# Kernel optimization log

Hardware: AMD Instinct MI355X
Metric: run time of the kernel (lower is better)

## Reference

```python
import jax, jax.numpy as jnp
import numpy as np

B, L, D, H, PD = 1, 512, 1024, 16, 128
HW = D // H  # 64


def _layernorm(x, g, b, eps=1e-5):
    mu = jnp.mean(x, axis=-1, keepdims=True)
    var = jnp.var(x, axis=-1, keepdims=True)
    return (x - mu) * jax.lax.rsqrt(var + eps) * g + b


def setup_inputs() -> dict:
    key = jax.random.key(0)
    ks = jax.random.split(key, 16)
    s = 0.02
    return {
        "sequence_state": jax.random.normal(ks[0], (B, L, D), jnp.float32),
        "pairwise_state": jax.random.normal(ks[1], (B, L, L, PD), jnp.float32),
        "mask": jnp.ones((B, L), dtype=bool),
        # layernorm before attention
        "ln1_g": jnp.ones((D,), jnp.float32),
        "ln1_b": jnp.zeros((D,), jnp.float32),
        # attention params (weights stored [in, out])
        "proj_w": jax.random.normal(ks[2], (D, 3 * H * HW), jnp.float32) * s,
        "g_w": jax.random.normal(ks[3], (D, H * HW), jnp.float32) * s,
        "g_b": jnp.ones((H * HW,), jnp.float32),
        "o_w": jax.random.normal(ks[4], (H * HW, D), jnp.float32) * s,
        "o_b": jnp.zeros((D,), jnp.float32),
        # pair-to-sequence bias
        "p2s_ln_g": jnp.ones((PD,), jnp.float32),
        "p2s_ln_b": jnp.zeros((PD,), jnp.float32),
        "p2s_w": jax.random.normal(ks[5], (PD, H), jnp.float32) * s,
        # residue MLP
        "mlp_ln_g": jnp.ones((D,), jnp.float32),
        "mlp_ln_b": jnp.zeros((D,), jnp.float32),
        "mlp_w1": jax.random.normal(ks[6], (D, 4 * D), jnp.float32) * s,
        "mlp_b1": jnp.zeros((4 * D,), jnp.float32),
        "mlp_w2": jax.random.normal(ks[7], (4 * D, D), jnp.float32) * s,
        "mlp_b2": jnp.zeros((D,), jnp.float32),
    }


def reference(sequence_state, pairwise_state, mask,
              ln1_g, ln1_b, proj_w, g_w, g_b, o_w, o_b,
              p2s_ln_g, p2s_ln_b, p2s_w,
              mlp_ln_g, mlp_ln_b, mlp_w1, mlp_b1, mlp_w2, mlp_b2):
    # PairToSequence: LN over pairwise feature dim, then project to per-head bias
    z = _layernorm(pairwise_state, p2s_ln_g, p2s_ln_b)
    bias = jnp.einsum("bqkp,ph->bhqk", z, p2s_w)  # [B,H,L,L]

    # Pre-attention layernorm
    y = _layernorm(sequence_state, ln1_g, ln1_b)

    # Gated attention with pairwise bias
    t = (y @ proj_w).reshape(B, L, H, 3 * HW)
    q, k, v = jnp.split(t, 3, axis=-1)  # each [B,L,H,HW]
    q = q * (HW ** -0.5)
    a = jnp.einsum("bqhc,bkhc->bhqk", q, k) + bias
    a = jnp.where(mask[:, None, None, :], a, -jnp.inf)
    a = jax.nn.softmax(a, axis=-1)
    o = jnp.einsum("bhqk,bkhc->bqhc", a, v).reshape(B, L, H * HW)
    gate = jax.nn.sigmoid(y @ g_w + g_b)
    o = (gate * o) @ o_w + o_b

    # residual (dropout=0 -> identity)
    s = sequence_state + o

    # ResidueMLP: x + Linear(ReLU(Linear(LN(x))))
    h = _layernorm(s, mlp_ln_g, mlp_ln_b)
    h = jax.nn.relu(h @ mlp_w1 + mlp_b1) @ mlp_w2 + mlp_b2
    return s + h
```

## Files before the change

kernel.cpp:

```cpp
#include <hip/hip_runtime.h>


typedef __attribute__((ext_vector_type(8))) short bfrag;
typedef __attribute__((ext_vector_type(4))) float f32x4;
typedef unsigned short ushort_t;
typedef unsigned int u32;

#define AS1 __attribute__((address_space(1)))
#define AS3 __attribute__((address_space(3)))

__device__ __forceinline__ void gll16(const void* g, void* l) {
  __builtin_amdgcn_global_load_lds((const AS1 u32*)g, (AS3 u32*)l, 16, 0, 0);
}

__device__ __forceinline__ unsigned short f2b(float x) {
  union { float f; unsigned u; } a; a.f = x;
  unsigned r = a.u + 0x7fffu + ((a.u >> 16) & 1u);
  return (unsigned short)(r >> 16);
}
__device__ __forceinline__ unsigned pack2(float a, float b) {
  return (unsigned)f2b(a) | ((unsigned)f2b(b) << 16);
}
__device__ __forceinline__ float b2f(ushort_t u) {
  union { float f; unsigned v; } a; a.v = ((unsigned)u) << 16; return a.f;
}

#define OFF_BIASH ((size_t)0)
#define OFF_Y     ((size_t)8388608)
#define OFF_QS    (OFF_Y    + (size_t)1048576)
#define OFF_KS    (OFF_QS   + (size_t)1048576)
#define OFF_VT    (OFF_KS   + (size_t)1048576)
#define OFF_GATE  (OFF_VT   + (size_t)1048576)
#define OFF_OG    (OFF_GATE + (size_t)2097152)
#define OFF_S     (OFF_OG   + (size_t)1048576)
#define OFF_HLN   (OFF_S    + (size_t)2097152)
#define OFF_H1    (OFF_HLN  + (size_t)1048576)
#define OFF_WPG   (OFF_H1   + (size_t)4194304)
#define OFF_WO    (OFF_WPG  + (size_t)8388608)
#define OFF_W1    (OFF_WO   + (size_t)2097152)
#define OFF_W2    (OFF_W1   + (size_t)8388608)

__device__ __forceinline__ void transp_tile(
    const float* __restrict__ W, ushort_t* __restrict__ Wt, int K, int N,
    int bx, int by, int tid, float* smem) {
  float (*tile)[65] = (float(*)[65])smem;
  int n0 = bx * 64, k0 = by * 64;
  int tr = tid >> 4, tc = (tid & 15) * 4;
#pragma unroll
  for (int i = 0; i < 4; i++) {
    int r = tr + i * 16;
    f32x4 v = __builtin_nontemporal_load(
        (const f32x4*)&W[(long)(k0 + r) * N + n0 + tc]);
    tile[r][tc] = v.x; tile[r][tc + 1] = v.y; tile[r][tc + 2] = v.z; tile[r][tc + 3] = v.w;
  }
  __syncthreads();
  int nr = tid >> 2, kk = (tid & 3) * 16;
  ushort_t* dst = Wt + (long)(n0 + nr) * K + k0 + kk;
  uint4 q;
  q.x = pack2(tile[kk + 0][nr], tile[kk + 1][nr]);
  q.y = pack2(tile[kk + 2][nr], tile[kk + 3][nr]);
  q.z = pack2(tile[kk + 4][nr], tile[kk + 5][nr]);
  q.w = pack2(tile[kk + 6][nr], tile[kk + 7][nr]);
  *(uint4*)dst = q;
  uint4 q2;
  q2.x = pack2(tile[kk + 8][nr],  tile[kk + 9][nr]);
  q2.y = pack2(tile[kk + 10][nr], tile[kk + 11][nr]);
  q2.z = pack2(tile[kk + 12][nr], tile[kk + 13][nr]);
  q2.w = pack2(tile[kk + 14][nr], tile[kk + 15][nr]);
  *(uint4*)(dst + 8) = q2;
}

__global__ __launch_bounds__(256) void mega1(
    const float* __restrict__ pw,
    const float* __restrict__ p2s_g, const float* __restrict__ p2s_b,
    const float* __restrict__ p2s_w,
    const float* __restrict__ proj_w, const float* __restrict__ g_w,
    const float* __restrict__ o_w, const float* __restrict__ w1,
    const float* __restrict__ w2,
    const float* __restrict__ seq, const float* __restrict__ ln1_g,
    const float* __restrict__ ln1_b, const float* __restrict__ o_b,
    ushort_t* __restrict__ biasH, ushort_t* __restrict__ wpg,
    ushort_t* __restrict__ wo, ushort_t* __restrict__ w1t,
    ushort_t* __restrict__ w2t, ushort_t* __restrict__ ybf,
    float* __restrict__ sbuf) {
  __shared__ float smemF[5920];
  const int id = blockIdx.x, t = threadIdx.x;

  if (id < 4096) {
    ushort_t* wb  = (ushort_t*)smemF;
    ushort_t* zsb = wb + 2048;
    ushort_t* res = zsb + 64 * 136;
    const int w = t >> 6, lane = t & 63, ln = lane & 15, quad = lane >> 4;
    const long pair0 = (long)id * 64;
    const int p = w * 16 + (lane >> 2);
    const int j = lane & 3;

#pragma unroll
    for (int i = t; i < 2048; i += 256) {
      int f = i >> 4, hh = i & 15;
      int chunk = f >> 5, q2 = (f >> 3) & 3, jj = f & 7;
      wb[(chunk * 64 + q2 * 16 + hh) * 8 + jj] = f2b(p2s_w[i]);
    }

    const float* xbase = pw + (pair0 + p) * 128 + j * 4;
    f32x4 xv[8];
#pragma unroll
    for (int q = 0; q < 8; q++)
      xv[q] = __builtin_nontemporal_load((const f32x4*)(xbase + q * 16));
    float s = 0.f, sq = 0.f;
#pragma unroll
    for (int q = 0; q < 8; q++) {
      s  += xv[q].x + xv[q].y + xv[q].z + xv[q].w;
      sq += xv[q].x*xv[q].x + xv[q].y*xv[q].y + xv[q].z*xv[q].z + xv[q].w*xv[q].w;
    }
    s += __shfl_xor(s, 1); s += __shfl_xor(s, 2);
    sq += __shfl_xor(sq, 1); sq += __shfl_xor(sq, 2);
    float mu = s * (1.f / 128.f);
    float rs = rsqrtf(sq * (1.f / 128.f) - mu * mu + 1e-5f);

#pragma unroll
    for (int q = 0; q < 8; q++) {
      f32x4 gv = *(const f32x4*)(p2s_g + j * 4 + q * 16);
      f32x4 bv = *(const f32x4*)(p2s_b + j * 4 + q * 16);
      uint2 o;
      o.x = pack2((xv[q].x - mu) * rs * gv.x + bv.x, (xv[q].y - mu) * rs * gv.y + bv.y);
      o.y = pack2((xv[q].z - mu) * rs * gv.z + bv.z, (xv[q].w - mu) * rs * gv.w + bv.w);
      *(uint2*)&zsb[p * 136 + q * 16 + j * 4] = o;
    }
    __syncthreads();

    f32x4 acc = (f32x4){0.f, 0.f, 0.f, 0.f};
#pragma unroll
    for (int chunk = 0; chunk < 4; chunk++) {
      bfrag a  = *(const bfrag*)&zsb[(w * 16 + ln) * 136 + chunk * 32 + quad * 8];
      bfrag bf = *(const bfrag*)&wb[(chunk * 64 + quad * 16 + ln) * 8];
      acc = __builtin_amdgcn_mfma_f32_16x16x32_bf16(a, bf, acc, 0, 0, 0);
    }
    *(uint2*)&res[ln * 68 + w * 16 + quad * 4] =
        (uint2){pack2(acc[0], acc[1]), pack2(acc[2], acc[3])};
    __syncthreads();
    {
      int hh = t >> 4, base = (t & 15) * 4;
      *(uint2*)&biasH[(long)hh * 262144 + pair0 + base] =
          *(const uint2*)&res[hh * 68 + base];
    }
  } else if (id < 7424) {
    int j = id - 4096;
    if (j < 768)       transp_tile(proj_w, wpg, 1024, 3072, j % 48, j / 48, t, smemF);
    else if (j < 1024) { j -= 768;  transp_tile(g_w, wpg + (long)3072 * 1024, 1024, 1024, j % 16, j / 16, t, smemF); }
    else if (j < 1280) { j -= 1024; transp_tile(o_w, wo, 1024, 1024, j % 16, j / 16, t, smemF); }
    else if (j < 2304) { j -= 1280; transp_tile(w1, w1t, 1024, 4096, j % 64, j / 64, t, smemF); }
    else               { j -= 2304; transp_tile(w2, w2t, 4096, 1024, j % 16, j / 16, t, smemF); }
  } else {
    int row = id - 7424;
    long base = (long)row * 1024 + t * 4;
    float4 v = *(const float4*)(seq + base);
    float4 ob = *(const float4*)(o_b + t * 4);
    float4 sv; sv.x = v.x + ob.x; sv.y = v.y + ob.y; sv.z = v.z + ob.z; sv.w = v.w + ob.w;
    *(float4*)(sbuf + base) = sv;
    float s  = v.x + v.y + v.z + v.w;
    float sq = v.x*v.x + v.y*v.y + v.z*v.z + v.w*v.w;
#pragma unroll
    for (int k = 1; k < 64; k <<= 1) { s += __shfl_xor(s, k); sq += __shfl_xor(sq, k); }
    if ((t & 63) == 0) { smemF[t >> 6] = s; smemF[4 + (t >> 6)] = sq; }
    __syncthreads();
    s  = smemF[0] + smemF[1] + smemF[2] + smemF[3];
    sq = smemF[4] + smemF[5] + smemF[6] + smemF[7];
    float mu = s * (1.f / 1024.f);
    float rsd = rsqrtf(sq * (1.f / 1024.f) - mu * mu + 1e-5f);
    float4 gv = *(const float4*)(ln1_g + t * 4);
    float4 bv = *(const float4*)(ln1_b + t * 4);
    uint2 o;
    o.x = pack2((v.x - mu) * rsd * gv.x + bv.x, (v.y - mu) * rsd * gv.y + bv.y);
    o.y = pack2((v.z - mu) * rsd * gv.z + bv.z, (v.w - mu) * rsd * gv.w + bv.w);
    *(uint2*)(ybf + base) = o;
  }
}

template <int EPI>
__global__ __launch_bounds__(256) void gemm64(
    const ushort_t* __restrict__ A, const ushort_t* __restrict__ Bt,
    int lda, int ldb, int Ksplit,
    const float* __restrict__ bias1,
    float* __restrict__ outF, ushort_t* __restrict__ outH, int ldc,
    ushort_t* __restrict__ qs, ushort_t* __restrict__ ks,
    ushort_t* __restrict__ vt, float* __restrict__ gatebuf) {
  __shared__ ushort_t As[2][64 * 32];
  __shared__ ushort_t Bs[2][64 * 32];
  const int tid = threadIdx.x;
  const int w = tid >> 6, lane = tid & 63;
  const int ln = lane & 15, quad = lane >> 4;
  const int wm = w >> 1, wn = w & 1;
  const int m0 = blockIdx.y * 64, n0 = blockIdx.x * 64;
  const int z = blockIdx.z;
  const int Koff = (EPI == 7) ? z * Ksplit : 0;

  const ushort_t* ga = A  + (long)(m0 + (tid >> 2)) * lda + Koff + (tid & 3) * 8;
  const ushort_t* gb = Bt + (long)(n0 + (tid >> 2)) * ldb + Koff + (tid & 3) * 8;
  unsigned wofs = __builtin_amdgcn_readfirstlane(w * 1024);
  char* lA[2] = {(char*)&As[0][0] + wofs, (char*)&As[1][0] + wofs};
  char* lB[2] = {(char*)&Bs[0][0] + wofs, (char*)&Bs[1][0] + wofs};

  f32x4 acc[2][2];
#pragma unroll
  for (int i = 0; i < 2; i++)
#pragma unroll
    for (int jj = 0; jj < 2; jj++) acc[i][jj] = (f32x4){0.f, 0.f, 0.f, 0.f};

  gll16(ga, lA[0]);
  gll16(gb, lB[0]);
  int buf = 0;
  for (int k0 = 0; k0 < Ksplit; k0 += 32) {
    __syncthreads();
    if (k0 + 32 < Ksplit) {
      gll16(ga + k0 + 32, lA[buf ^ 1]);
      gll16(gb + k0 + 32, lB[buf ^ 1]);
    }
    const ushort_t* Ab = &As[buf][0];
    const ushort_t* Bb = &Bs[buf][0];
    bfrag a0 = *(const bfrag*)&Ab[(wm * 32 + ln) * 32 + quad * 8];
    bfrag a1 = *(const bfrag*)&Ab[(wm * 32 + 16 + ln) * 32 + quad * 8];
    bfrag b0 = *(const bfrag*)&Bb[(wn * 32 + ln) * 32 + quad * 8];
    bfrag b1 = *(const bfrag*)&Bb[(wn * 32 + 16 + ln) * 32 + quad * 8];
    acc[0][0] = __builtin_amdgcn_mfma_f32_16x16x32_bf16(a0, b0, acc[0][0], 0, 0, 0);
    acc[0][1] = __builtin_amdgcn_mfma_f32_16x16x32_bf16(a0, b1, acc[0][1], 0, 0, 0);
    acc[1][0] = __builtin_amdgcn_mfma_f32_16x16x32_bf16(a1, b0, acc[1][0], 0, 0, 0);
    acc[1][1] = __builtin_amdgcn_mfma_f32_16x16x32_bf16(a1, b1, acc[1][1], 0, 0, 0);
    buf ^= 1;
  }

#pragma unroll
  for (int am = 0; am < 2; am++) {
#pragma unroll
    for (int bn = 0; bn < 2; bn++) {
      int ocol = n0 + wn * 32 + bn * 16 + ln;
#pragma unroll
      for (int r = 0; r < 4; r++) {
        int orow = m0 + wm * 32 + am * 16 + quad * 4 + r;
        float v = acc[am][bn][r];
        if (EPI == 3) {
          v = fmaxf(v + bias1[ocol], 0.f);
          outH[(long)orow * ldc + ocol] = f2b(v);
        } else if (EPI == 6) {
          if (ocol < 3072) {
            int h = ocol / 192, jq = ocol - h * 192;
            if (jq < 64)       qs[((long)h * 512 + orow) * 64 + jq] = f2b(v * 0.125f);
            else if (jq < 128) ks[((long)h * 512 + orow) * 64 + (jq - 64)] = f2b(v);
            else               vt[((long)h * 64 + (jq - 128)) * 512 + orow] = f2b(v);
          } else {
            int gcol = ocol - 3072;
            float gv = v + bias1[gcol];
            gatebuf[(long)orow * 1024 + gcol] = 1.f / (1.f + __expf(-gv));
          }
        } else {
          atomicAdd(&outF[(long)orow * ldc + ocol], v);
        }
      }
    }
  }
}

__global__ __launch_bounds__(256) void flash_attn(
    const ushort_t* __restrict__ qs, const ushort_t* __restrict__ ks,
    const ushort_t* __restrict__ vt, const ushort_t* __restrict__ biasH,
    const float* __restrict__ gate, ushort_t* __restrict__ og) {
  __shared__ ushort_t Qs[32 * 72];
  __shared__ ushort_t Ks[64 * 72];
  __shared__ ushort_t Vs[64 * 72];
  __shared__ ushort_t Ps[4][16 * 40];
  const int tid = threadIdx.x;
  const int w = tid >> 6, lane = tid & 63, ln = lane & 15, quad = lane >> 4;
  const int wm = w >> 1, wn = w & 1;
  const int h = blockIdx.x, q0 = blockIdx.y * 32;

  { int r = tid >> 3, c = (tid & 7) * 8;
    *(uint4*)&Qs[r * 72 + c] = *(const uint4*)(qs + ((long)(h * 512 + q0 + r)) * 64 + c); }

  float m_[4], l_[4];
  f32x4 Oacc[4];
#pragma unroll
  for (int i = 0; i < 4; i++) { m_[i] = -1e30f; l_[i] = 0.f; Oacc[i] = (f32x4){0.f,0.f,0.f,0.f}; }

  const int rkv = tid >> 2, ckv = (tid & 3) * 16;

  for (int kt = 0; kt < 8; kt++) {
    const int k0 = kt * 64;
    __syncthreads();
    { const ushort_t* sk = ks + ((long)(h * 512 + k0 + rkv)) * 64 + ckv;
      *(uint4*)&Ks[rkv * 72 + ckv]     = *(const uint4*)sk;
      *(uint4*)&Ks[rkv * 72 + ckv + 8] = *(const uint4*)(sk + 8);
      const ushort_t* sv = vt + ((long)(h * 64 + rkv)) * 512 + k0 + ckv;
      *(uint4*)&Vs[rkv * 72 + ckv]     = *(const uint4*)sv;
      *(uint4*)&Vs[rkv * 72 + ckv + 8] = *(const uint4*)(sv + 8); }

    f32x4 acc[2];
    const ushort_t* bp = biasH + ((long)(h * 512 + q0 + wm * 16 + quad * 4)) * 512
                         + k0 + wn * 32 + ln;
#pragma unroll
    for (int t4 = 0; t4 < 2; t4++)
#pragma unroll
      for (int rr = 0; rr < 4; rr++)
        acc[t4][rr] = b2f(bp[(long)rr * 512 + t4 * 16]);

    __syncthreads();
#pragma unroll
    for (int s = 0; s < 2; s++) {
      bfrag a = *(const bfrag*)&Qs[(wm * 16 + ln) * 72 + s * 32 + quad * 8];
#pragma unroll
      for (int t4 = 0; t4 < 2; t4++) {
        bfrag b = *(const bfrag*)&Ks[(wn * 32 + t4 * 16 + ln) * 72 + s * 32 + quad * 8];
        acc[t4] = __builtin_amdgcn_mfma_f32_16x16x32_bf16(a, b, acc[t4], 0, 0, 0);
      }
    }

    float mt[4];
#pragma unroll
    for (int rr = 0; rr < 4; rr++) mt[rr] = fmaxf(acc[0][rr], acc[1][rr]);
#pragma unroll
    for (int xm = 1; xm < 16; xm <<= 1)
#pragma unroll
      for (int rr = 0; rr < 4; rr++) mt[rr] = fmaxf(mt[rr], __shfl_xor(mt[rr], xm));
    float al[4];
#pragma unroll
    for (int rr = 0; rr < 4; rr++) {
      float mn = fmaxf(m_[rr], mt[rr]);
      al[rr] = __expf(m_[rr] - mn);
      m_[rr] = mn;
    }
#pragma unroll
    for (int t4 = 0; t4 < 2; t4++)
#pragma unroll
      for (int rr = 0; rr < 4; rr++)
        acc[t4][rr] = __expf(acc[t4][rr] - m_[rr]);
    float rsl[4];
#pragma unroll
    for (int rr = 0; rr < 4; rr++) rsl[rr] = acc[0][rr] + acc[1][rr];
#pragma unroll
    for (int xm = 1; xm < 16; xm <<= 1)
#pragma unroll
      for (int rr = 0; rr < 4; rr++) rsl[rr] += __shfl_xor(rsl[rr], xm);
#pragma unroll
    for (int rr = 0; rr < 4; rr++) l_[rr] = l_[rr] * al[rr] + rsl[rr];
#pragma unroll
    for (int t4 = 0; t4 < 4; t4++)
#pragma unroll
      for (int rr = 0; rr < 4; rr++) Oacc[t4][rr] *= al[rr];

#pragma unroll
    for (int t4 = 0; t4 < 2; t4++)
#pragma unroll
      for (int rr = 0; rr < 4; rr++)
        Ps[w][(quad * 4 + rr) * 40 + t4 * 16 + ln] = f2b(acc[t4][rr]);
    __builtin_amdgcn_wave_barrier();
    __builtin_amdgcn_s_waitcnt(0xC07F);
    __builtin_amdgcn_wave_barrier();

    {
      bfrag a = *(const bfrag*)&Ps[w][ln * 40 + quad * 8];
#pragma unroll
      for (int t4 = 0; t4 < 4; t4++) {
        bfrag b = *(const bfrag*)&Vs[(t4 * 16 + ln) * 72 + wn * 32 + quad * 8];
        Oacc[t4] = __builtin_amdgcn_mfma_f32_16x16x32_bf16(a, b, Oacc[t4], 0, 0, 0);
      }
    }
  }

  __syncthreads();
  float* ml = (float*)(void*)Ks;
  if (ln == 0)
#pragma unroll
    for (int rr = 0; rr < 4; rr++) {
      ml[(w * 16 + quad * 4 + rr) * 2 + 0] = m_[rr];
      ml[(w * 16 + quad * 4 + rr) * 2 + 1] = l_[rr];
    }
  __syncthreads();
  const int pw_ = wm * 2 + (wn ^ 1);
  float a_self[4];
#pragma unroll
  for (int rr = 0; rr < 4; rr++) {
    float mo = ml[(pw_ * 16 + quad * 4 + rr) * 2 + 0];
    float lo = ml[(pw_ * 16 + quad * 4 + rr) * 2 + 1];
    float mF = fmaxf(m_[rr], mo);
    a_self[rr] = __expf(m_[rr] - mF);
    l_[rr] = l_[rr] * a_self[rr] + lo * __expf(mo - mF);
  }
  float* Of = (float*)(void*)Vs;
  if (wn == 1) {
#pragma unroll
    for (int t4 = 0; t4 < 4; t4++)
#pragma unroll
      for (int rr = 0; rr < 4; rr++)
        Of[(wm * 16 + quad * 4 + rr) * 68 + t4 * 16 + ln] = Oacc[t4][rr] * a_self[rr];
  }
  __syncthreads();
  if (wn == 0) {
#pragma unroll
    for (int t4 = 0; t4 < 4; t4++) {
#pragma unroll
      for (int rr = 0; rr < 4; rr++) {
        int grow = q0 + wm * 16 + quad * 4 + rr;
        int gcol = h * 64 + t4 * 16 + ln;
        float v = Oacc[t4][rr] * a_self[rr]
                + Of[(wm * 16 + quad * 4 + rr) * 68 + t4 * 16 + ln];
        v /= l_[rr];
        og[(long)grow * 1024 + gcol] = f2b(v * gate[(long)grow * 1024 + gcol]);
      }
    }
  }
}

__global__ __launch_bounds__(256) void ln2(
    const float* __restrict__ sbuf, const float* __restrict__ g,
    const float* __restrict__ b, const float* __restrict__ b2,
    ushort_t* __restrict__ hln, float* __restrict__ out) {
  __shared__ float ps[8];
  int row = blockIdx.x, t = threadIdx.x;
  long base = (long)row * 1024 + t * 4;
  float4 v = *(const float4*)(sbuf + base);
  float4 b2v = *(const float4*)(b2 + t * 4);
  float4 ov; ov.x = v.x + b2v.x; ov.y = v.y + b2v.y; ov.z = v.z + b2v.z; ov.w = v.w + b2v.w;
  *(float4*)(out + base) = ov;
  float s  = v.x + v.y + v.z + v.w;
  float sq = v.x*v.x + v.y*v.y + v.z*v.z + v.w*v.w;
#pragma unroll
  for (int k = 1; k < 64; k <<= 1) { s += __shfl_xor(s, k); sq += __shfl_xor(sq, k); }
  if ((t & 63) == 0) { ps[t >> 6] = s; ps[4 + (t >> 6)] = sq; }
  __syncthreads();
  s  = ps[0] + ps[1] + ps[2] + ps[3];
  sq = ps[4] + ps[5] + ps[6] + ps[7];
  float mu = s * (1.f / 1024.f);
  float rsd = rsqrtf(sq * (1.f / 1024.f) - mu * mu + 1e-5f);
  float4 gv = *(const float4*)(g + t * 4);
  float4 bv = *(const float4*)(b + t * 4);
  uint2 o;
  o.x = pack2((v.x - mu) * rsd * gv.x + bv.x, (v.y - mu) * rsd * gv.y + bv.y);
  o.y = pack2((v.z - mu) * rsd * gv.z + bv.z, (v.w - mu) * rsd * gv.w + bv.w);
  *(uint2*)(hln + base) = o;
}

extern "C" void kernel_launch(void* const* d_in, const int* in_sizes, int n_in,
                              void* d_out, int out_size, void* d_ws, size_t ws_size,
                              hipStream_t stream) {
  const float* seq    = (const float*)d_in[0];
  const float* pw     = (const float*)d_in[1];
  const float* ln1_g  = (const float*)d_in[3];
  const float* ln1_b  = (const float*)d_in[4];
  const float* proj_w = (const float*)d_in[5];
  const float* g_w    = (const float*)d_in[6];
  const float* g_b    = (const float*)d_in[7];
  const float* o_w    = (const float*)d_in[8];
  const float* o_b    = (const float*)d_in[9];
  const float* p2s_g  = (const float*)d_in[10];
  const float* p2s_b  = (const float*)d_in[11];
  const float* p2s_w  = (const float*)d_in[12];
  const float* mlp_g  = (const float*)d_in[13];
  const float* mlp_bb = (const float*)d_in[14];
  const float* w1     = (const float*)d_in[15];
  const float* b1     = (const float*)d_in[16];
  const float* w2     = (const float*)d_in[17];
  const float* b2     = (const float*)d_in[18];
  float* out = (float*)d_out;
  char* ws = (char*)d_ws;

  ushort_t* biasH = (ushort_t*)(ws + OFF_BIASH);
  ushort_t* ybf   = (ushort_t*)(ws + OFF_Y);
  ushort_t* qs    = (ushort_t*)(ws + OFF_QS);
  ushort_t* ks    = (ushort_t*)(ws + OFF_KS);
  ushort_t* vt    = (ushort_t*)(ws + OFF_VT);
  float* gatebuf  = (float*)(ws + OFF_GATE);
  ushort_t* og    = (ushort_t*)(ws + OFF_OG);
  float* sbuf     = (float*)(ws + OFF_S);
  ushort_t* hln   = (ushort_t*)(ws + OFF_HLN);
  ushort_t* h1    = (ushort_t*)(ws + OFF_H1);
  ushort_t* wpg   = (ushort_t*)(ws + OFF_WPG);
  ushort_t* wo    = (ushort_t*)(ws + OFF_WO);
  ushort_t* w1t   = (ushort_t*)(ws + OFF_W1);
  ushort_t* w2t   = (ushort_t*)(ws + OFF_W2);

  mega1<<<7936, 256, 0, stream>>>(pw, p2s_g, p2s_b, p2s_w,
                                  proj_w, g_w, o_w, w1, w2,
                                  seq, ln1_g, ln1_b, o_b,
                                  biasH, wpg, wo, w1t, w2t, ybf, sbuf);
  gemm64<6><<<dim3(64, 8, 1), 256, 0, stream>>>(ybf, wpg, 1024, 1024, 1024,
                                                g_b, nullptr, nullptr, 0,
                                                qs, ks, vt, gatebuf);
  flash_attn<<<dim3(16, 16), 256, 0, stream>>>(qs, ks, vt, biasH, gatebuf, og);
  gemm64<7><<<dim3(16, 8, 4), 256, 0, stream>>>(og, wo, 1024, 1024, 256,
                                                nullptr, sbuf, nullptr, 1024,
                                                nullptr, nullptr, nullptr, nullptr);
  ln2<<<512, 256, 0, stream>>>(sbuf, mlp_g, mlp_bb, b2, hln, out);
  gemm64<3><<<dim3(64, 8, 1), 256, 0, stream>>>(hln, w1t, 1024, 1024, 1024,
                                                b1, nullptr, h1, 4096,
                                                nullptr, nullptr, nullptr, nullptr);
  gemm64<7><<<dim3(16, 8, 4), 256, 0, stream>>>(h1, w2t, 4096, 4096, 1024,
                                                nullptr, out, nullptr, 1024,
                                                nullptr, nullptr, nullptr, nullptr);
}
```

Before: 330.3 us.

## Deepen gemm64 LDS pipeline to four stages with explicit vmcnt waits

Replaces the double-buffered LDS staging in the generic 64x64 GEMM with a four-slot ring that keeps three K-tiles of global-to-LDS loads in flight. It synchronises with explicit s_waitcnt vmcnt counters and raw s_barrier instead of __syncthreads. The goal is to hide more global memory latency behind the MFMA work. In exchange it doubles the LDS footprint, which may reduce occupancy, and it relies on hand-counted outstanding loads, which is fragile if the compiler reorders or adds memory ops.

```diff
diff --git a/kernel.cpp b/kernel.cpp
--- a/kernel.cpp
+++ b/kernel.cpp
@@ -185,8 +185,8 @@
     float* __restrict__ outF, ushort_t* __restrict__ outH, int ldc,
     ushort_t* __restrict__ qs, ushort_t* __restrict__ ks,
     ushort_t* __restrict__ vt, float* __restrict__ gatebuf) {
-  __shared__ ushort_t As[2][64 * 32];
-  __shared__ ushort_t Bs[2][64 * 32];
+  __shared__ ushort_t As[4][64 * 32];
+  __shared__ ushort_t Bs[4][64 * 32];
   const int tid = threadIdx.x;
   const int w = tid >> 6, lane = tid & 63;
   const int ln = lane & 15, quad = lane >> 4;
@@ -198,8 +198,8 @@
   const ushort_t* ga = A  + (long)(m0 + (tid >> 2)) * lda + Koff + (tid & 3) * 8;
   const ushort_t* gb = Bt + (long)(n0 + (tid >> 2)) * ldb + Koff + (tid & 3) * 8;
   unsigned wofs = __builtin_amdgcn_readfirstlane(w * 1024);
-  char* lA[2] = {(char*)&As[0][0] + wofs, (char*)&As[1][0] + wofs};
-  char* lB[2] = {(char*)&Bs[0][0] + wofs, (char*)&Bs[1][0] + wofs};
+  char* lAw = (char*)&As[0][0] + wofs;
+  char* lBw = (char*)&Bs[0][0] + wofs;
 
   f32x4 acc[2][2];
 #pragma unroll
@@ -207,17 +207,14 @@
 #pragma unroll
     for (int jj = 0; jj < 2; jj++) acc[i][jj] = (f32x4){0.f, 0.f, 0.f, 0.f};
 
-  gll16(ga, lA[0]);
-  gll16(gb, lB[0]);
-  int buf = 0;
-  for (int k0 = 0; k0 < Ksplit; k0 += 32) {
-    __syncthreads();
-    if (k0 + 32 < Ksplit) {
-      gll16(ga + k0 + 32, lA[buf ^ 1]);
-      gll16(gb + k0 + 32, lB[buf ^ 1]);
-    }
-    const ushort_t* Ab = &As[buf][0];
-    const ushort_t* Bb = &Bs[buf][0];
+  auto stage = [&](int t) {
+    int boff = (t & 3) * 4096;
+    gll16(ga + t * 32, lAw + boff);
+    gll16(gb + t * 32, lBw + boff);
+  };
+  auto body = [&](int b) {
+    const ushort_t* Ab = (const ushort_t*)((const char*)&As[0][0] + b * 4096);
+    const ushort_t* Bb = (const ushort_t*)((const char*)&Bs[0][0] + b * 4096);
     bfrag a0 = *(const bfrag*)&Ab[(wm * 32 + ln) * 32 + quad * 8];
     bfrag a1 = *(const bfrag*)&Ab[(wm * 32 + 16 + ln) * 32 + quad * 8];
     bfrag b0 = *(const bfrag*)&Bb[(wn * 32 + ln) * 32 + quad * 8];
@@ -226,7 +223,27 @@
     acc[0][1] = __builtin_amdgcn_mfma_f32_16x16x32_bf16(a0, b1, acc[0][1], 0, 0, 0);
     acc[1][0] = __builtin_amdgcn_mfma_f32_16x16x32_bf16(a1, b0, acc[1][0], 0, 0, 0);
     acc[1][1] = __builtin_amdgcn_mfma_f32_16x16x32_bf16(a1, b1, acc[1][1], 0, 0, 0);
-    buf ^= 1;
+  };
+
+  const int niter = Ksplit >> 5;
+  stage(0);
+  if (niter > 1) stage(1);
+  if (niter > 2) stage(2);
+
+  int k = 0;
+  for (; k + 2 < niter; ++k) {
+    asm volatile("s_waitcnt vmcnt(4)" ::: "memory");
+    __builtin_amdgcn_s_barrier();
+    __builtin_amdgcn_sched_barrier(0);
+    if (k + 3 < niter) stage(k + 3);
+    body(k & 3);
+  }
+  for (; k < niter; ++k) {
+    if (k + 1 < niter) { asm volatile("s_waitcnt vmcnt(2)" ::: "memory"); }
+    else               { asm volatile("s_waitcnt vmcnt(0)" ::: "memory"); }
+    __builtin_amdgcn_s_barrier();
+    __builtin_amdgcn_sched_barrier(0);
+    body(k & 3);
   }
 
 #pragma unroll
```

After: 332.8 us. No clear change (+0.8%).
